# Optimization experiments

Measured on AMD Instinct MI355X. Metric: run time of the kernel, lower is better.

## Reference

```python
import jax, jax.numpy as jnp
import numpy as np

N = 100_000      # nodes
E = 3_200_000    # edges (avg degree 32)
F_IN = 100       # raw feature dim (embedding Linear(100, 64))
H = 64           # in/hidden/out channels
C = 18           # class_num
EPS = 1e-12      # F.normalize eps


def _sage_conv(x, src, dst, edge_weight, Wl, bl, Wr):
    """PyG-style SAGEConv: mean-aggregate neighbor messages, two linears, L2 normalize."""
    msg = x[src]                                   # [E, d] gather of x_j
    if edge_weight is not None:
        msg = msg * edge_weight[:, None]
    agg = jax.ops.segment_sum(msg, dst, num_segments=N)                       # [N, d]
    deg = jax.ops.segment_sum(jnp.ones((src.shape[0],), x.dtype), dst, num_segments=N)
    mean = agg / jnp.maximum(deg, 1.0)[:, None]
    out = mean @ Wl + bl + x @ Wr                  # lin_l(aggr) + lin_r(root)
    nrm = jnp.sqrt(jnp.sum(out * out, axis=-1, keepdims=True))
    return out / jnp.maximum(nrm, EPS)


def setup_inputs() -> dict:
    key = jax.random.key(0)
    ks = jax.random.split(key, 16)
    s = 0.1
    inp = {
        "x": jax.random.normal(ks[0], (N, F_IN), jnp.float32),
        "edge_index": jax.random.randint(ks[1], (2, E), 0, N, dtype=jnp.int64),
        "edge_weight": jax.random.uniform(ks[2], (E,), jnp.float32),
        "emb_W": jax.random.normal(ks[3], (F_IN, H), jnp.float32) * s,
        "emb_b": jnp.zeros((H,), jnp.float32),
    }
    k = 4
    for i in (1, 2, 3):
        inp[f"Wl{i}"] = jax.random.normal(ks[k], (H, H), jnp.float32) * s; k += 1
        inp[f"bl{i}"] = jnp.zeros((H,), jnp.float32)
        inp[f"Wr{i}"] = jax.random.normal(ks[k], (H, H), jnp.float32) * s; k += 1
    inp["Wl4"] = jax.random.normal(ks[k], (H, C), jnp.float32) * s; k += 1
    inp["bl4"] = jnp.zeros((C,), jnp.float32)
    inp["Wr4"] = jax.random.normal(ks[k], (H, C), jnp.float32) * s
    return inp


def reference(x, edge_index, edge_weight, emb_W, emb_b,
              Wl1, bl1, Wr1, Wl2, bl2, Wr2, Wl3, bl3, Wr3,
              Wl4, bl4, Wr4):
    src, dst = edge_index[0], edge_index[1]
    h = jax.nn.relu(x @ emb_W + emb_b)             # embedding MLP
    for Wl, bl, Wr in ((Wl1, bl1, Wr1), (Wl2, bl2, Wr2), (Wl3, bl3, Wr3)):
        h = jax.nn.relu(_sage_conv(h, src, dst, edge_weight, Wl, bl, Wr))
        # dropout p=0.2 is identity in eval mode
    return _sage_conv(h, src, dst, None, Wl4, bl4, Wr4)
```

## Files before the change

### kernel.cpp

```cpp
#include <hip/hip_runtime.h>
#include <hip/hip_bf16.h>

#define N_NODES   100000
#define N_EDGES   3200000
#define F_IN      100
#define H_DIM     64
#define C_NUM     18
#define NPB       256
#define N_BKT     391
#define EPB       8192
#define N_TILES   1563

typedef __attribute__((ext_vector_type(8))) short short8;
typedef __attribute__((ext_vector_type(4))) float f32x4;
typedef __attribute__((ext_vector_type(2))) float f32x2;

__device__ __forceinline__ float ldf(const void* p, long long i, int isbf) {
    if (isbf) return __bfloat162float(((const __hip_bfloat16*)p)[i]);
    return ((const float*)p)[i];
}
__device__ __forceinline__ int ldi(const void* p, long long i, int is64) {
    if (is64) return (int)(((const long long*)p)[i]);
    return ((const int*)p)[i];
}
__device__ __forceinline__ unsigned short f2us(float f) {
    __hip_bfloat16 b = __float2bfloat16(f);
    return *(unsigned short*)&b;
}
__device__ __forceinline__ unsigned char f2fp8(float f) {
    int p = __builtin_amdgcn_cvt_pk_fp8_f32(f, 0.0f, 0, false);
    return (unsigned char)(p & 0xFF);
}

__global__ void detect_kernel(const void* ei, const void* x, int* flags)
{
    if (blockIdx.x != 0 || threadIdx.x >= 64) return;
    const int lane = threadIdx.x;
    const long long* e64 = (const long long*)ei;
    int bad = 0;
#pragma unroll
    for (int i = lane; i < 128; i += 64) {
        long long v = e64[i];
        if (v < 0 || v >= N_NODES) bad = 1;
    }
    unsigned long long anybad = __ballot(bad);
    const __hip_bfloat16* xb = (const __hip_bfloat16*)x;
    int cnt = 0;
#pragma unroll
    for (int i = lane; i < 256; i += 64) {
        float v = fabsf(__bfloat162float(xb[i]));
        if (v == 0.0f || (v > 9.5367431640625e-7f && v < 1.0e6f)) ++cnt;
    }
#pragma unroll
    for (int m = 1; m <= 32; m <<= 1) cnt += __shfl_xor(cnt, m);
    if (lane == 0) {
        flags[0] = (anybad == 0ULL) ? 1 : 0;
        flags[1] = (cnt >= 240) ? 1 : 0;
    }
}

__global__ void zero_cnt(int* __restrict__ pcnt)
{
    int i = threadIdx.x;
    if (i < N_BKT) pcnt[i] = 0;
}

__global__ __launch_bounds__(1024) void radix_count(const void* ei, int* __restrict__ pcnt,
                                                    const int* __restrict__ flags)
{
    __shared__ int hist[N_BKT];
    const int t = threadIdx.x;
    if (t < N_BKT) hist[t] = 0;
    __syncthreads();
    const int base = blockIdx.x * EPB;
    const int n = min(EPB, N_EDGES - base);
    const int is64 = flags[0];
    for (int j = t; j < n; j += 1024) {
        int d = ldi(ei, (long long)N_EDGES + base + j, is64);
        atomicAdd(&hist[d >> 8], 1);
    }
    __syncthreads();
    if (t < N_BKT) atomicAdd(&pcnt[t], hist[t]);
}

__global__ void scan_bkt(const int* __restrict__ cnt, int* __restrict__ base,
                         int* __restrict__ cursor)
{
    __shared__ int tmp[512];
    const int t = threadIdx.x;
    int v = (t < N_BKT) ? cnt[t] : 0;
    tmp[t] = v;
    __syncthreads();
    for (int off = 1; off < 512; off <<= 1) {
        int add = (t >= off) ? tmp[t - off] : 0;
        __syncthreads();
        tmp[t] += add;
        __syncthreads();
    }
    if (t < N_BKT) { base[t] = tmp[t] - v; cursor[t] = tmp[t] - v; }
    if (t == 511) base[N_BKT] = tmp[511];
}

__global__ __launch_bounds__(1024) void radix_scatter(const void* ei, const void* ew,
                                                      int* __restrict__ gcursor,
                                                      uint2* __restrict__ temp,
                                                      const int* __restrict__ flags)
{
    __shared__ uint2 stage[EPB];
    __shared__ int hist[512], scan_s[512];
    __shared__ int gbase[N_BKT], lcur[N_BKT];
    const int t = threadIdx.x;
    if (t < 512) hist[t] = 0;
    __syncthreads();

    const int base = blockIdx.x * EPB;
    const int n = min(EPB, N_EDGES - base);
    const int is64 = flags[0], isbf = flags[1];

    int  bkt[8];
    uint2 pk[8];
#pragma unroll
    for (int j = 0; j < 8; ++j) {
        int i = j * 1024 + t;
        bkt[j] = -1;
        if (i < n) {
            int e = base + i;
            int s = ldi(ei, e, is64);
            int d = ldi(ei, (long long)N_EDGES + e, is64);
            float w = ldf(ew, e, isbf);
            bkt[j] = d >> 8;
            pk[j].x = (unsigned)s | ((unsigned)(d & (NPB - 1)) << 17);
            pk[j].y = (unsigned)f2us(w) | ((unsigned)bkt[j] << 16);
            atomicAdd(&hist[bkt[j]], 1);
        }
    }
    __syncthreads();
    if (t < 512) scan_s[t] = hist[t];
    __syncthreads();
    for (int off = 1; off < 512; off <<= 1) {
        int add = 0;
        if (t < 512 && t >= off) add = scan_s[t - off];
        __syncthreads();
        if (t < 512) scan_s[t] += add;
        __syncthreads();
    }
    if (t < N_BKT) {
        int excl = scan_s[t] - hist[t];
        lcur[t] = excl;
        gbase[t] = atomicAdd(&gcursor[t], hist[t]) - excl;
    }
    __syncthreads();
#pragma unroll
    for (int j = 0; j < 8; ++j) {
        if (bkt[j] >= 0) {
            int pos = atomicAdd(&lcur[bkt[j]], 1);
            stage[pos] = pk[j];
        }
    }
    __syncthreads();
#pragma unroll
    for (int j = 0; j < 8; ++j) {
        int i = j * 1024 + t;
        if (i < n) {
            int b = (int)(stage[i].y >> 16);
            temp[gbase[b] + i] = stage[i];
        }
    }
}

__global__ __launch_bounds__(256) void csr_build(const uint2* __restrict__ temp,
                          const int* __restrict__ pbase,
                          unsigned int* __restrict__ csr_pk,
                          int* __restrict__ deg, int* __restrict__ row_start,
                          float* __restrict__ inv_deg)
{
    __shared__ int cnt[NPB], scan_s[NPB], cur[NPB];
    const int b = blockIdx.x;
    const int t = threadIdx.x;
    cnt[t] = 0;
    __syncthreads();
    const int bs = pbase[b];
    const int be = pbase[b + 1];
    for (int i = bs + t; i < be; i += NPB)
        atomicAdd(&cnt[(temp[i].x >> 17) & (NPB - 1)], 1);
    __syncthreads();
    int v = cnt[t];
    scan_s[t] = v;
    __syncthreads();
    for (int off = 1; off < NPB; off <<= 1) {
        int add = (t >= off) ? scan_s[t - off] : 0;
        __syncthreads();
        scan_s[t] += add;
        __syncthreads();
    }
    int excl = bs + scan_s[t] - v;
    cur[t] = excl;
    int node = b * NPB + t;
    if (node < N_NODES) {
        deg[node]       = v;
        row_start[node] = excl;
        inv_deg[node]   = 1.0f / (float)max(v, 1);
    }
    __syncthreads();
    for (int i = bs + t; i < be; i += NPB) {
        uint2 e = temp[i];
        int k = (e.x >> 17) & (NPB - 1);
        int pos = atomicAdd(&cur[k], 1);
        csr_pk[pos] = (e.x & 0x1FFFFu) | ((e.y & 0x7FFFu) << 17);
    }
}

template <int CP, int COUT>
__device__ __forceinline__ void stage_W(unsigned short* W_s, const void* Wl, const void* Wr,
                                        int t, int isbf)
{
    constexpr int KP = 136;
    const int n0 = t >> 3, k8a = t & 7;
    for (int n = n0; n < CP; n += 32) {
#pragma unroll
        for (int hh = 0; hh < 2; ++hh) {
            int k8 = k8a + hh * 8;
            union { unsigned short u[8]; short8 v; } tmp;
#pragma unroll
            for (int j = 0; j < 8; ++j) {
                int k = k8 * 8 + j;
                float val = 0.0f;
                if (n < COUT && k < 128)
                    val = (k < 64) ? ldf(Wl, (long long)k * COUT + n, isbf)
                                   : ldf(Wr, (long long)(k - 64) * COUT + n, isbf);
                tmp.u[j] = f2us(val);
            }
            *(short8*)&W_s[n * KP + k8 * 8] = tmp.v;
        }
    }
}

__global__ void embed_mfma(const void* x, const void* W, const void* b,
                           __hip_bfloat16* __restrict__ h,
                           unsigned char* __restrict__ h8,
                           const int* __restrict__ flags)
{
    constexpr int KP = 136;
    __shared__ unsigned short W_s[H_DIM * KP];
    __shared__ unsigned short x_s[64 * KP];
    __shared__ float b_s[H_DIM];
    const int t = threadIdx.x;
    const int isbf = flags[1];

    {
        const int n0 = t >> 3, k8a = t & 7;
        for (int n = n0; n < H_DIM; n += 32) {
#pragma unroll
            for (int hh = 0; hh < 2; ++hh) {
                int k8 = k8a + hh * 8;
                union { unsigned short u[8]; short8 v; } tmp;
#pragma unroll
                for (int j = 0; j < 8; ++j) {
                    int k = k8 * 8 + j;
                    tmp.u[j] = (k < F_IN) ? f2us(ldf(W, (long long)k * H_DIM + n, isbf))
                                          : (unsigned short)0;
                }
                *(short8*)&W_s[n * KP + k8 * 8] = tmp.v;
            }
        }
    }
    if (t < H_DIM) b_s[t] = ldf(b, t, isbf);
    for (int i = t; i < 64 * 36; i += 256) {
        int row = i / 36, col = 100 + (i % 36);
        x_s[row * KP + col] = 0;
    }

    const int wave = t >> 6, lane = t & 63, c = lane & 15, quad = lane >> 4;

    for (int tile = blockIdx.x; tile < N_TILES; tile += gridDim.x) {
        const int nb0 = tile * 64;
        const int valid = min(64, N_NODES - nb0);
        __syncthreads();
        if (isbf) {
            const uint2* xu = (const uint2*)x + (size_t)nb0 * 25;
            for (int i2 = t; i2 < valid * 25; i2 += 256) {
                int row = i2 / 25, col4 = i2 - row * 25;
                *(uint2*)&x_s[row * KP + col4 * 4] = xu[i2];
            }
        } else {
            for (int i = t; i < valid * 100; i += 256) {
                int row = i / 100, col = i - row * 100;
                x_s[row * KP + col] = f2us(((const float*)x)[(size_t)(nb0 + row) * 100 + col]);
            }
        }
        if (valid < 64) {
            for (int i = t; i < (64 - valid) * 100; i += 256) {
                int row = valid + i / 100, col = i % 100;
                x_s[row * KP + col] = 0;
            }
        }
        __syncthreads();

        short8 bfrag[4][4];
#pragma unroll
        for (int nt = 0; nt < 4; ++nt)
#pragma unroll
            for (int kt = 0; kt < 4; ++kt)
                bfrag[nt][kt] = *(const short8*)&W_s[(nt * 16 + c) * KP + kt * 32 + quad * 8];

        short8 afrag[4];
#pragma unroll
        for (int kt = 0; kt < 4; ++kt)
            afrag[kt] = *(const short8*)&x_s[(wave * 16 + c) * KP + kt * 32 + quad * 8];

        f32x4 acc[4] = {};
#pragma unroll
        for (int nt = 0; nt < 4; ++nt)
#pragma unroll
            for (int kt = 0; kt < 4; ++kt)
                acc[nt] = __builtin_amdgcn_mfma_f32_16x16x32_bf16(afrag[kt], bfrag[nt][kt], acc[nt], 0, 0, 0);

        const int nb = nb0 + wave * 16;
#pragma unroll
        for (int nt = 0; nt < 4; ++nt)
#pragma unroll
            for (int reg = 0; reg < 4; ++reg) {
                int nn = nb + quad * 4 + reg;
                int col = nt * 16 + c;
                if (nn < N_NODES) {
                    float v = fmaxf(acc[nt][reg] + b_s[col], 0.0f);
                    h[(size_t)nn * H_DIM + col] = __float2bfloat16(v);
                    h8[(size_t)nn * H_DIM + col] = f2fp8(v);
                }
            }
    }
}

#define ACC16(HV, W) do {                                                          \
    f32x2 f_;                                                                      \
    f_ = __builtin_amdgcn_cvt_pk_f32_fp8((int)HV.x, false); a[0]=fmaf(W,f_.x,a[0]);  a[1]=fmaf(W,f_.y,a[1]);   \
    f_ = __builtin_amdgcn_cvt_pk_f32_fp8((int)HV.x, true ); a[2]=fmaf(W,f_.x,a[2]);  a[3]=fmaf(W,f_.y,a[3]);   \
    f_ = __builtin_amdgcn_cvt_pk_f32_fp8((int)HV.y, false); a[4]=fmaf(W,f_.x,a[4]);  a[5]=fmaf(W,f_.y,a[5]);   \
    f_ = __builtin_amdgcn_cvt_pk_f32_fp8((int)HV.y, true ); a[6]=fmaf(W,f_.x,a[6]);  a[7]=fmaf(W,f_.y,a[7]);   \
    f_ = __builtin_amdgcn_cvt_pk_f32_fp8((int)HV.z, false); a[8]=fmaf(W,f_.x,a[8]);  a[9]=fmaf(W,f_.y,a[9]);   \
    f_ = __builtin_amdgcn_cvt_pk_f32_fp8((int)HV.z, true ); a[10]=fmaf(W,f_.x,a[10]); a[11]=fmaf(W,f_.y,a[11]); \
    f_ = __builtin_amdgcn_cvt_pk_f32_fp8((int)HV.w, false); a[12]=fmaf(W,f_.x,a[12]); a[13]=fmaf(W,f_.y,a[13]); \
    f_ = __builtin_amdgcn_cvt_pk_f32_fp8((int)HV.w, true ); a[14]=fmaf(W,f_.x,a[14]); a[15]=fmaf(W,f_.y,a[15]); \
} while (0)

template <bool USE_W>
__global__ __launch_bounds__(256) void gather_mean(const unsigned char* __restrict__ h8,
                            const unsigned int* __restrict__ csr_pk,
                            const int* __restrict__ row_start,
                            const int* __restrict__ deg,
                            const float* __restrict__ inv_deg,
                            __hip_bfloat16* __restrict__ mean)
{
    const int lane = threadIdx.x & 63;
    const int c4 = lane & 3;
    const int r4 = lane >> 2;
    const int wid = blockIdx.x * 4 + (threadIdx.x >> 6);
    const int nw  = gridDim.x * 4;

    for (int n = wid; n < N_NODES; n += nw) {
        const int s0 = row_start[n];
        const int d0 = deg[n];
        unsigned int ev = (lane < d0) ? csr_pk[s0 + lane] : 0u;
        const int m0 = min(d0, 64);
        float a[16] = {};

        for (int j0 = 0; j0 < m0; j0 += 32) {
            unsigned int eA = __shfl(ev, j0 + r4);
            unsigned int eB = __shfl(ev, j0 + 16 + r4);
            uint4 hvA = *(const uint4*)(h8 + (size_t)(eA & 0x1FFFF) * H_DIM + 16 * c4);
            uint4 hvB = *(const uint4*)(h8 + (size_t)(eB & 0x1FFFF) * H_DIM + 16 * c4);
            float wA, wB;
            if (USE_W) {
                wA = __uint_as_float((eA & 0xFFFE0000u) >> 1);
                wB = __uint_as_float((eB & 0xFFFE0000u) >> 1);
            } else {
                wA = (j0 + r4 < m0) ? 1.0f : 0.0f;
                wB = (j0 + 16 + r4 < m0) ? 1.0f : 0.0f;
            }
            ACC16(hvA, wA);
            ACC16(hvB, wB);
        }
        for (int jb = 64; jb < d0; jb += 16) {
            int j = jb + r4;
            unsigned int e2 = (j < d0) ? csr_pk[s0 + j] : 0u;
            float w;
            if (USE_W) w = __uint_as_float((e2 & 0xFFFE0000u) >> 1);
            else       w = (j < d0) ? 1.0f : 0.0f;
            uint4 hv = *(const uint4*)(h8 + (size_t)(e2 & 0x1FFFF) * H_DIM + 16 * c4);
            ACC16(hv, w);
        }

#pragma unroll
        for (int i = 0; i < 8; ++i) {
            float keep = (lane & 4) ? a[i + 8] : a[i];
            float give = (lane & 4) ? a[i] : a[i + 8];
            a[i] = keep + __shfl_xor(give, 4);
        }
#pragma unroll
        for (int i = 0; i < 4; ++i) {
            float keep = (lane & 8) ? a[i + 4] : a[i];
            float give = (lane & 8) ? a[i] : a[i + 4];
            a[i] = keep + __shfl_xor(give, 8);
        }
#pragma unroll
        for (int i = 0; i < 2; ++i) {
            float keep = (lane & 16) ? a[i + 2] : a[i];
            float give = (lane & 16) ? a[i] : a[i + 2];
            a[i] = keep + __shfl_xor(give, 16);
        }
        {
            float keep = (lane & 32) ? a[1] : a[0];
            float give = (lane & 32) ? a[0] : a[1];
            a[0] = keep + __shfl_xor(give, 32);
        }
        const int f = c4 * 16 + ((lane >> 2) & 1) * 8 + ((lane >> 3) & 1) * 4
                    + ((lane >> 4) & 1) * 2 + ((lane >> 5) & 1);
        mean[(size_t)n * H_DIM + f] = __float2bfloat16(a[0] * inv_deg[n]);
    }
}

template <int COUT, bool RELU, bool FINAL>
__global__ void transform_mfma(const __hip_bfloat16* __restrict__ meanp,
                               const __hip_bfloat16* __restrict__ hp,
                               const void* Wl, const void* bl, const void* Wr,
                               __hip_bfloat16* __restrict__ h_out,
                               unsigned char* __restrict__ h8_out,
                               const int* __restrict__ flags, void* dout)
{
    constexpr int CP = (COUT + 15) & ~15;
    constexpr int NT = CP / 16;
    constexpr int KP = 136;
    __shared__ unsigned short W_s[CP * KP];
    __shared__ float b_s[CP];
    const int t = threadIdx.x;
    const int isbf = flags[1];
    stage_W<CP, COUT>(W_s, Wl, Wr, t, isbf);
    if (t < CP) b_s[t] = (t < COUT) ? ldf(bl, t, isbf) : 0.0f;
    __syncthreads();

    const int wave = t >> 6, lane = t & 63, c = lane & 15, quad = lane >> 4;
    short8 bfrag[NT][4];
#pragma unroll
    for (int nt = 0; nt < NT; ++nt)
#pragma unroll
        for (int kt = 0; kt < 4; ++kt)
            bfrag[nt][kt] = *(const short8*)&W_s[(nt * 16 + c) * KP + kt * 32 + quad * 8];

    for (int tile = blockIdx.x; tile < N_TILES; tile += gridDim.x) {
        const int nbw = tile * 64 + wave * 16;
        if (nbw >= N_NODES) continue;
        int node = nbw + c; if (node >= N_NODES) node = N_NODES - 1;

        short8 afrag[4];
#pragma unroll
        for (int kt = 0; kt < 4; ++kt) {
            const __hip_bfloat16* sp = (kt < 2) ? meanp : hp;
            afrag[kt] = *(const short8*)(sp + (size_t)node * H_DIM + (kt & 1) * 32 + quad * 8);
        }

        f32x4 acc[NT] = {};
#pragma unroll
        for (int nt = 0; nt < NT; ++nt)
#pragma unroll
            for (int kt = 0; kt < 4; ++kt)
                acc[nt] = __builtin_amdgcn_mfma_f32_16x16x32_bf16(afrag[kt], bfrag[nt][kt], acc[nt], 0, 0, 0);

        float rs[4];
#pragma unroll
        for (int reg = 0; reg < 4; ++reg) {
            float s2 = 0.f;
#pragma unroll
            for (int nt = 0; nt < NT; ++nt) {
                float v = acc[nt][reg] + b_s[nt * 16 + c];
                acc[nt][reg] = v;
                s2 += v * v;
            }
            s2 += __shfl_xor(s2, 1); s2 += __shfl_xor(s2, 2);
            s2 += __shfl_xor(s2, 4); s2 += __shfl_xor(s2, 8);
            rs[reg] = 1.0f / fmaxf(sqrtf(s2), 1e-12f);
        }

#pragma unroll
        for (int nt = 0; nt < NT; ++nt)
#pragma unroll
            for (int reg = 0; reg < 4; ++reg) {
                int nn  = nbw + quad * 4 + reg;
                int col = nt * 16 + c;
                if (nn < N_NODES && col < COUT) {
                    float v = acc[nt][reg] * rs[reg];
                    if (RELU) v = fmaxf(v, 0.0f);
                    if (FINAL) {
                        if (isbf) ((__hip_bfloat16*)dout)[(size_t)nn * COUT + col] = __float2bfloat16(v);
                        else      ((float*)dout)[(size_t)nn * COUT + col] = v;
                    } else {
                        h_out[(size_t)nn * H_DIM + col] = __float2bfloat16(v);
                        h8_out[(size_t)nn * H_DIM + col] = f2fp8(v);
                    }
                }
            }
    }
}

extern "C" void kernel_launch(void* const* d_in, const int* in_sizes, int n_in,
                              void* d_out, int out_size, void* d_ws, size_t ws_size,
                              hipStream_t stream)
{
    const void* x    = d_in[0];
    const void* ei   = d_in[1];
    const void* ew   = d_in[2];
    const void* embW = d_in[3];
    const void* embB = d_in[4];
    const void* Wl1 = d_in[5];  const void* bl1 = d_in[6];  const void* Wr1 = d_in[7];
    const void* Wl2 = d_in[8];  const void* bl2 = d_in[9];  const void* Wr2 = d_in[10];
    const void* Wl3 = d_in[11]; const void* bl3 = d_in[12]; const void* Wr3 = d_in[13];
    const void* Wl4 = d_in[14]; const void* bl4 = d_in[15]; const void* Wr4 = d_in[16];
    (void)in_sizes; (void)n_in; (void)out_size; (void)ws_size;

    char* ws = (char*)d_ws;
    size_t off = 0;
    auto alloc = [&](size_t bytes) -> void* {
        void* p = ws + off;
        off += (bytes + 255) & ~(size_t)255;
        return p;
    };
    uint2* temp = (uint2*)alloc((size_t)N_EDGES * sizeof(uint2));
    __hip_bfloat16* hA = (__hip_bfloat16*)temp;
    __hip_bfloat16* hB = (__hip_bfloat16*)((char*)temp + (size_t)N_NODES * H_DIM * 2);
    unsigned int* csr_pk = (unsigned int*)alloc((size_t)N_EDGES * sizeof(unsigned int));
    __hip_bfloat16* mn = (__hip_bfloat16*)alloc((size_t)N_NODES * H_DIM * 2);
    unsigned char* h8 = (unsigned char*)alloc((size_t)N_NODES * H_DIM);
    int*   pcnt    = (int*)  alloc((N_BKT)     * sizeof(int));
    int*   pbase   = (int*)  alloc((N_BKT + 1) * sizeof(int));
    int*   pcursor = (int*)  alloc((N_BKT)     * sizeof(int));
    int*   deg     = (int*)  alloc((size_t)N_NODES * sizeof(int));
    int*   row_st  = (int*)  alloc((size_t)N_NODES * sizeof(int));
    float* inv_deg = (float*)alloc((size_t)N_NODES * sizeof(float));
    int*   flags   = (int*)  alloc(256);

    const int NBr = (N_EDGES + EPB - 1) / EPB;

    detect_kernel<<<1, 64, 0, stream>>>(ei, x, flags);
    zero_cnt<<<1, 512, 0, stream>>>(pcnt);
    radix_count<<<NBr, 1024, 0, stream>>>(ei, pcnt, flags);
    scan_bkt<<<1, 512, 0, stream>>>(pcnt, pbase, pcursor);
    radix_scatter<<<NBr, 1024, 0, stream>>>(ei, ew, pcursor, temp, flags);
    csr_build<<<N_BKT, NPB, 0, stream>>>(temp, pbase, csr_pk, deg, row_st, inv_deg);

    embed_mfma<<<512, 256, 0, stream>>>(x, embW, embB, hA, h8, flags);

    gather_mean<true><<<2048, 256, 0, stream>>>(h8, csr_pk, row_st, deg, inv_deg, mn);
    transform_mfma<H_DIM, true, false><<<512, 256, 0, stream>>>(
        mn, hA, Wl1, bl1, Wr1, hB, h8, flags, d_out);
    gather_mean<true><<<2048, 256, 0, stream>>>(h8, csr_pk, row_st, deg, inv_deg, mn);
    transform_mfma<H_DIM, true, false><<<512, 256, 0, stream>>>(
        mn, hB, Wl2, bl2, Wr2, hA, h8, flags, d_out);
    gather_mean<true><<<2048, 256, 0, stream>>>(h8, csr_pk, row_st, deg, inv_deg, mn);
    transform_mfma<H_DIM, true, false><<<512, 256, 0, stream>>>(
        mn, hA, Wl3, bl3, Wr3, hB, h8, flags, d_out);
    gather_mean<false><<<2048, 256, 0, stream>>>(h8, csr_pk, row_st, deg, inv_deg, mn);
    transform_mfma<C_NUM, false, true><<<512, 256, 0, stream>>>(
        mn, hB, Wl4, bl4, Wr4, nullptr, nullptr, flags, d_out);
}
```

Baseline: 520.6 us.

## Fuse neighbor gather-mean with MFMA transform into one per-layer kernel

Merges the gather_mean and transform_mfma kernels into a single sage_layer kernel. Each block aggregates 64 nodes into shared memory and then runs the bf16 MFMA linear, normalize and ReLU on them, so the global mean buffer round trip and one launch per layer go away. Each wave now prefetches the next node's CSR edge entries, and the fp8 feature buffer is double-buffered so reads and writes of h8 do not race within one kernel. In exchange, every block restages the weights (1563 blocks instead of 512), and the per-block node count is fixed, which can lower load balance against the previous grid-stride gather.

```diff
diff --git a/kernel.cpp b/kernel.cpp
--- a/kernel.cpp
+++ b/kernel.cpp
@@ -343,25 +343,63 @@
     f_ = __builtin_amdgcn_cvt_pk_f32_fp8((int)HV.w, true ); a[14]=fmaf(W,f_.x,a[14]); a[15]=fmaf(W,f_.y,a[15]); \
 } while (0)
 
-template <bool USE_W>
-__global__ __launch_bounds__(256) void gather_mean(const unsigned char* __restrict__ h8,
-                            const unsigned int* __restrict__ csr_pk,
-                            const int* __restrict__ row_start,
-                            const int* __restrict__ deg,
-                            const float* __restrict__ inv_deg,
-                            __hip_bfloat16* __restrict__ mean)
-{
-    const int lane = threadIdx.x & 63;
-    const int c4 = lane & 3;
-    const int r4 = lane >> 2;
-    const int wid = blockIdx.x * 4 + (threadIdx.x >> 6);
-    const int nw  = gridDim.x * 4;
-
-    for (int n = wid; n < N_NODES; n += nw) {
-        const int s0 = row_start[n];
-        const int d0 = deg[n];
-        unsigned int ev = (lane < d0) ? csr_pk[s0 + lane] : 0u;
-        const int m0 = min(d0, 64);
+template <int COUT, bool RELU, bool FINAL, bool USE_W>
+__global__ __launch_bounds__(256) void sage_layer(
+        const __hip_bfloat16* __restrict__ hp,
+        const unsigned char* __restrict__ h8,
+        const unsigned int* __restrict__ csr_pk,
+        const int* __restrict__ row_start,
+        const int* __restrict__ deg,
+        const float* __restrict__ inv_deg,
+        const void* Wl, const void* bl, const void* Wr,
+        __hip_bfloat16* __restrict__ h_out,
+        unsigned char* __restrict__ h8_out,
+        const int* __restrict__ flags, void* dout)
+{
+    constexpr int CP = (COUT + 15) & ~15;
+    constexpr int NT = CP / 16;
+    constexpr int KP = 136;
+    constexpr int MP = 72;
+    __shared__ unsigned short W_s[CP * KP];
+    __shared__ unsigned short mean_s[64 * MP];
+    __shared__ float b_s[CP];
+    const int t = threadIdx.x;
+    const int isbf = flags[1];
+    stage_W<CP, COUT>(W_s, Wl, Wr, t, isbf);
+    if (t < CP) b_s[t] = (t < COUT) ? ldf(bl, t, isbf) : 0.0f;
+    __syncthreads();
+
+    const int wave = t >> 6, lane = t & 63, c = lane & 15, quad = lane >> 4;
+    const int c4 = lane & 3, r4 = lane >> 2;
+
+    short8 bfrag[NT][4];
+#pragma unroll
+    for (int nt = 0; nt < NT; ++nt)
+#pragma unroll
+        for (int kt = 0; kt < 4; ++kt)
+            bfrag[nt][kt] = *(const short8*)&W_s[(nt * 16 + c) * KP + kt * 32 + quad * 8];
+
+    const int nb0 = blockIdx.x * 64;
+    const int wbase = nb0 + wave * 16;
+
+    int sA = 0, dA = 0;
+    {
+        int nn = wbase + lane;
+        if (lane < 16 && nn < N_NODES) { sA = row_start[nn]; dA = deg[nn]; }
+    }
+    int s0 = __shfl(sA, 0), d0 = __shfl(dA, 0);
+    unsigned int ev_next = (lane < d0) ? csr_pk[s0 + lane] : 0u;
+
+    for (int i = 0; i < 16; ++i) {
+        const int n = wbase + i;
+        unsigned int ev = ev_next;
+        const int dcur = __shfl(dA, i);
+        if (i < 15) {
+            int s1 = __shfl(sA, i + 1), d1 = __shfl(dA, i + 1);
+            ev_next = (lane < d1) ? csr_pk[s1 + lane] : 0u;
+        }
+        if (n >= N_NODES) continue;
+        const int m0 = min(dcur, 64);
         float a[16] = {};
 
         for (int j0 = 0; j0 < m0; j0 += 32) {
@@ -380,33 +418,33 @@
             ACC16(hvA, wA);
             ACC16(hvB, wB);
         }
-        for (int jb = 64; jb < d0; jb += 16) {
+        for (int jb = 64; jb < dcur; jb += 16) {
             int j = jb + r4;
-            unsigned int e2 = (j < d0) ? csr_pk[s0 + j] : 0u;
+            unsigned int e2 = (j < dcur) ? csr_pk[__shfl(sA, i) + j] : 0u;
             float w;
             if (USE_W) w = __uint_as_float((e2 & 0xFFFE0000u) >> 1);
-            else       w = (j < d0) ? 1.0f : 0.0f;
+            else       w = (j < dcur) ? 1.0f : 0.0f;
             uint4 hv = *(const uint4*)(h8 + (size_t)(e2 & 0x1FFFF) * H_DIM + 16 * c4);
             ACC16(hv, w);
         }
 
 #pragma unroll
-        for (int i = 0; i < 8; ++i) {
-            float keep = (lane & 4) ? a[i + 8] : a[i];
-            float give = (lane & 4) ? a[i] : a[i + 8];
-            a[i] = keep + __shfl_xor(give, 4);
-        }
-#pragma unroll
-        for (int i = 0; i < 4; ++i) {
-            float keep = (lane & 8) ? a[i + 4] : a[i];
-            float give = (lane & 8) ? a[i] : a[i + 4];
-            a[i] = keep + __shfl_xor(give, 8);
-        }
-#pragma unroll
-        for (int i = 0; i < 2; ++i) {
-            float keep = (lane & 16) ? a[i + 2] : a[i];
-            float give = (lane & 16) ? a[i] : a[i + 2];
-            a[i] = keep + __shfl_xor(give, 16);
+        for (int q = 0; q < 8; ++q) {
+            float keep = (lane & 4) ? a[q + 8] : a[q];
+            float give = (lane & 4) ? a[q] : a[q + 8];
+            a[q] = keep + __shfl_xor(give, 4);
+        }
+#pragma unroll
+        for (int q = 0; q < 4; ++q) {
+            float keep = (lane & 8) ? a[q + 4] : a[q];
+            float give = (lane & 8) ? a[q] : a[q + 4];
+            a[q] = keep + __shfl_xor(give, 8);
+        }
+#pragma unroll
+        for (int q = 0; q < 2; ++q) {
+            float keep = (lane & 16) ? a[q + 2] : a[q];
+            float give = (lane & 16) ? a[q] : a[q + 2];
+            a[q] = keep + __shfl_xor(give, 16);
         }
         {
             float keep = (lane & 32) ? a[1] : a[0];
@@ -415,90 +453,60 @@
         }
         const int f = c4 * 16 + ((lane >> 2) & 1) * 8 + ((lane >> 3) & 1) * 4
                     + ((lane >> 4) & 1) * 2 + ((lane >> 5) & 1);
-        mean[(size_t)n * H_DIM + f] = __float2bfloat16(a[0] * inv_deg[n]);
-    }
-}
-
-template <int COUT, bool RELU, bool FINAL>
-__global__ void transform_mfma(const __hip_bfloat16* __restrict__ meanp,
-                               const __hip_bfloat16* __restrict__ hp,
-                               const void* Wl, const void* bl, const void* Wr,
-                               __hip_bfloat16* __restrict__ h_out,
-                               unsigned char* __restrict__ h8_out,
-                               const int* __restrict__ flags, void* dout)
-{
-    constexpr int CP = (COUT + 15) & ~15;
-    constexpr int NT = CP / 16;
-    constexpr int KP = 136;
-    __shared__ unsigned short W_s[CP * KP];
-    __shared__ float b_s[CP];
-    const int t = threadIdx.x;
-    const int isbf = flags[1];
-    stage_W<CP, COUT>(W_s, Wl, Wr, t, isbf);
-    if (t < CP) b_s[t] = (t < COUT) ? ldf(bl, t, isbf) : 0.0f;
-    __syncthreads();
-
-    const int wave = t >> 6, lane = t & 63, c = lane & 15, quad = lane >> 4;
-    short8 bfrag[NT][4];
+        mean_s[(wave * 16 + i) * MP + f] = f2us(a[0] * inv_deg[n]);
+    }
+    __syncthreads();
+
+    const int nbw = wbase;
+    if (nbw >= N_NODES) return;
+    int node = nbw + c; if (node >= N_NODES) node = N_NODES - 1;
+
+    short8 afrag[4];
+    afrag[0] = *(const short8*)&mean_s[(wave * 16 + c) * MP + quad * 8];
+    afrag[1] = *(const short8*)&mean_s[(wave * 16 + c) * MP + 32 + quad * 8];
+    afrag[2] = *(const short8*)(hp + (size_t)node * H_DIM + quad * 8);
+    afrag[3] = *(const short8*)(hp + (size_t)node * H_DIM + 32 + quad * 8);
+
+    f32x4 acc[NT] = {};
 #pragma unroll
     for (int nt = 0; nt < NT; ++nt)
 #pragma unroll
         for (int kt = 0; kt < 4; ++kt)
-            bfrag[nt][kt] = *(const short8*)&W_s[(nt * 16 + c) * KP + kt * 32 + quad * 8];
-
-    for (int tile = blockIdx.x; tile < N_TILES; tile += gridDim.x) {
-        const int nbw = tile * 64 + wave * 16;
-        if (nbw >= N_NODES) continue;
-        int node = nbw + c; if (node >= N_NODES) node = N_NODES - 1;
-
-        short8 afrag[4];
-#pragma unroll
-        for (int kt = 0; kt < 4; ++kt) {
-            const __hip_bfloat16* sp = (kt < 2) ? meanp : hp;
-            afrag[kt] = *(const short8*)(sp + (size_t)node * H_DIM + (kt & 1) * 32 + quad * 8);
-        }
-
-        f32x4 acc[NT] = {};
-#pragma unroll
-        for (int nt = 0; nt < NT; ++nt)
-#pragma unroll
-            for (int kt = 0; kt < 4; ++kt)
-                acc[nt] = __builtin_amdgcn_mfma_f32_16x16x32_bf16(afrag[kt], bfrag[nt][kt], acc[nt], 0, 0, 0);
-
-        float rs[4];
+            acc[nt] = __builtin_amdgcn_mfma_f32_16x16x32_bf16(afrag[kt], bfrag[nt][kt], acc[nt], 0, 0, 0);
+
+    float rs[4];
+#pragma unroll
+    for (int reg = 0; reg < 4; ++reg) {
+        float s2 = 0.f;
+#pragma unroll
+        for (int nt = 0; nt < NT; ++nt) {
+            float v = acc[nt][reg] + b_s[nt * 16 + c];
+            acc[nt][reg] = v;
+            s2 += v * v;
+        }
+        s2 += __shfl_xor(s2, 1); s2 += __shfl_xor(s2, 2);
+        s2 += __shfl_xor(s2, 4); s2 += __shfl_xor(s2, 8);
+        rs[reg] = 1.0f / fmaxf(sqrtf(s2), 1e-12f);
+    }
+
+#pragma unroll
+    for (int nt = 0; nt < NT; ++nt)
 #pragma unroll
         for (int reg = 0; reg < 4; ++reg) {
-            float s2 = 0.f;
-#pragma unroll
-            for (int nt = 0; nt < NT; ++nt) {
-                float v = acc[nt][reg] + b_s[nt * 16 + c];
-                acc[nt][reg] = v;
-                s2 += v * v;
-            }
-            s2 += __shfl_xor(s2, 1); s2 += __shfl_xor(s2, 2);
-            s2 += __shfl_xor(s2, 4); s2 += __shfl_xor(s2, 8);
-            rs[reg] = 1.0f / fmaxf(sqrtf(s2), 1e-12f);
-        }
-
-#pragma unroll
-        for (int nt = 0; nt < NT; ++nt)
-#pragma unroll
-            for (int reg = 0; reg < 4; ++reg) {
-                int nn  = nbw + quad * 4 + reg;
-                int col = nt * 16 + c;
-                if (nn < N_NODES && col < COUT) {
-                    float v = acc[nt][reg] * rs[reg];
-                    if (RELU) v = fmaxf(v, 0.0f);
-                    if (FINAL) {
-                        if (isbf) ((__hip_bfloat16*)dout)[(size_t)nn * COUT + col] = __float2bfloat16(v);
-                        else      ((float*)dout)[(size_t)nn * COUT + col] = v;
-                    } else {
-                        h_out[(size_t)nn * H_DIM + col] = __float2bfloat16(v);
-                        h8_out[(size_t)nn * H_DIM + col] = f2fp8(v);
-                    }
+            int nn  = nbw + quad * 4 + reg;
+            int col = nt * 16 + c;
+            if (nn < N_NODES && col < COUT) {
+                float v = acc[nt][reg] * rs[reg];
+                if (RELU) v = fmaxf(v, 0.0f);
+                if (FINAL) {
+                    if (isbf) ((__hip_bfloat16*)dout)[(size_t)nn * COUT + col] = __float2bfloat16(v);
+                    else      ((float*)dout)[(size_t)nn * COUT + col] = v;
+                } else {
+                    h_out[(size_t)nn * H_DIM + col] = __float2bfloat16(v);
+                    h8_out[(size_t)nn * H_DIM + col] = f2fp8(v);
                 }
             }
-    }
+        }
 }
 
 extern "C" void kernel_launch(void* const* d_in, const int* in_sizes, int n_in,
@@ -527,8 +535,8 @@
     __hip_bfloat16* hA = (__hip_bfloat16*)temp;
     __hip_bfloat16* hB = (__hip_bfloat16*)((char*)temp + (size_t)N_NODES * H_DIM * 2);
     unsigned int* csr_pk = (unsigned int*)alloc((size_t)N_EDGES * sizeof(unsigned int));
-    __hip_bfloat16* mn = (__hip_bfloat16*)alloc((size_t)N_NODES * H_DIM * 2);
-    unsigned char* h8 = (unsigned char*)alloc((size_t)N_NODES * H_DIM);
+    unsigned char* h8A = (unsigned char*)alloc((size_t)N_NODES * H_DIM);
+    unsigned char* h8B = (unsigned char*)alloc((size_t)N_NODES * H_DIM);
     int*   pcnt    = (int*)  alloc((N_BKT)     * sizeof(int));
     int*   pbase   = (int*)  alloc((N_BKT + 1) * sizeof(int));
     int*   pcursor = (int*)  alloc((N_BKT)     * sizeof(int));
@@ -546,18 +554,14 @@
     radix_scatter<<<NBr, 1024, 0, stream>>>(ei, ew, pcursor, temp, flags);
     csr_build<<<N_BKT, NPB, 0, stream>>>(temp, pbase, csr_pk, deg, row_st, inv_deg);
 
-    embed_mfma<<<512, 256, 0, stream>>>(x, embW, embB, hA, h8, flags);
-
-    gather_mean<true><<<2048, 256, 0, stream>>>(h8, csr_pk, row_st, deg, inv_deg, mn);
-    transform_mfma<H_DIM, true, false><<<512, 256, 0, stream>>>(
-        mn, hA, Wl1, bl1, Wr1, hB, h8, flags, d_out);
-    gather_mean<true><<<2048, 256, 0, stream>>>(h8, csr_pk, row_st, deg, inv_deg, mn);
-    transform_mfma<H_DIM, true, false><<<512, 256, 0, stream>>>(
-        mn, hB, Wl2, bl2, Wr2, hA, h8, flags, d_out);
-    gather_mean<true><<<2048, 256, 0, stream>>>(h8, csr_pk, row_st, deg, inv_deg, mn);
-    transform_mfma<H_DIM, true, false><<<512, 256, 0, stream>>>(
-        mn, hA, Wl3, bl3, Wr3, hB, h8, flags, d_out);
-    gather_mean<false><<<2048, 256, 0, stream>>>(h8, csr_pk, row_st, deg, inv_deg, mn);
-    transform_mfma<C_NUM, false, true><<<512, 256, 0, stream>>>(
-        mn, hB, Wl4, bl4, Wr4, nullptr, nullptr, flags, d_out);
-}
+    embed_mfma<<<512, 256, 0, stream>>>(x, embW, embB, hA, h8A, flags);
+
+    sage_layer<H_DIM, true, false, true><<<N_TILES, 256, 0, stream>>>(
+        hA, h8A, csr_pk, row_st, deg, inv_deg, Wl1, bl1, Wr1, hB, h8B, flags, d_out);
+    sage_layer<H_DIM, true, false, true><<<N_TILES, 256, 0, stream>>>(
+        hB, h8B, csr_pk, row_st, deg, inv_deg, Wl2, bl2, Wr2, hA, h8A, flags, d_out);
+    sage_layer<H_DIM, true, false, true><<<N_TILES, 256, 0, stream>>>(
+        hA, h8A, csr_pk, row_st, deg, inv_deg, Wl3, bl3, Wr3, hB, h8B, flags, d_out);
+    sage_layer<C_NUM, false, true, false><<<N_TILES, 256, 0, stream>>>(
+        hB, h8B, csr_pk, row_st, deg, inv_deg, Wl4, bl4, Wr4, nullptr, nullptr, flags, d_out);
+}
```

Result: slower. 594.0 us (+14.1%).
